# Performance work log

Hardware: AMD Instinct MI355X
Metric: run time of the kernel (lower is better)

Reference implementation:

```python
import jax, jax.numpy as jnp
import numpy as np

T = 2048
C = 2048
N_HEAD = 16
HEAD_DIM = C // N_HEAD


def setup_inputs() -> dict:
    key = jax.random.key(0)
    k1, k2, k3 = jax.random.split(key, 3)
    x = jax.random.normal(k1, (T, C), dtype=jnp.float32)
    # eqx.nn.Linear weight convention: (out_features, in_features)
    W_attn = jax.random.normal(k2, (3 * C, C), dtype=jnp.float32) * (1.0 / np.sqrt(C))
    W_proj = jax.random.normal(k3, (C, C), dtype=jnp.float32) * (1.0 / np.sqrt(C))
    return {"x": x, "W_attn": W_attn, "W_proj": W_proj}


def reference(x, W_attn, W_proj):
    # qkv projection: (T, 3C)
    qkv = x @ W_attn.T
    q, k, v = jnp.split(qkv, 3, axis=-1)
    # reshape to (H, T, d)
    q = q.reshape(T, N_HEAD, HEAD_DIM).transpose(1, 0, 2)
    k = k.reshape(T, N_HEAD, HEAD_DIM).transpose(1, 0, 2)
    v = v.reshape(T, N_HEAD, HEAD_DIM).transpose(1, 0, 2)
    # scaled causal attention: (H, T, T)
    att = jnp.einsum('htd,hsd->hts', q, k)
    causal_mask = jnp.triu(jnp.ones((T, T), dtype=bool), k=1)  # mask future keys
    att = jnp.where(causal_mask, -jnp.inf, att)
    att = jax.nn.softmax(att / jnp.sqrt(jnp.float32(HEAD_DIM)), axis=-1)
    # attention output: (H, T, d) -> (T, C)
    out = jnp.einsum('hts,hsd->htd', att, v)
    out = out.transpose(1, 0, 2).reshape(T, C)
    return out @ W_proj.T
```

## Files before the change

kernel.cpp:

```cpp
#include <hip/hip_runtime.h>
#include <cstdint>

using bx8 = __attribute__((ext_vector_type(8))) __bf16;
using us8 = __attribute__((ext_vector_type(8))) unsigned short;
using us4 = __attribute__((ext_vector_type(4))) unsigned short;
using fl8 = __attribute__((ext_vector_type(8))) float;
using fx4 = __attribute__((ext_vector_type(4))) float;

static __device__ inline unsigned short f2bf(float f) {
  unsigned u = __builtin_bit_cast(unsigned, f);
  unsigned r = 0x7FFFu + ((u >> 16) & 1u);
  return (unsigned short)((u + r) >> 16);
}
static __device__ inline float bf2f(unsigned short s) {
  return __builtin_bit_cast(float, (unsigned)s << 16);
}

static __device__ inline fx4 mfma16(bx8 a, bx8 b, fx4 c) {
  return __builtin_amdgcn_mfma_f32_16x16x32_bf16(a, b, c, 0, 0, 0);
}

static __device__ inline void gload16(const void* g, void* lds) {
  __builtin_amdgcn_global_load_lds(
      (const __attribute__((address_space(1))) void*)g,
      (__attribute__((address_space(3))) void*)lds,
      16, 0, 0);
}
#define VMCNT(n) asm volatile("s_waitcnt vmcnt(" #n ")" ::: "memory")
static __device__ inline void wave_barrier() {
  __builtin_amdgcn_sched_barrier(0);
  __builtin_amdgcn_s_barrier();
  __builtin_amdgcn_sched_barrier(0);
}
static __device__ inline void lds_barrier() {
  __builtin_amdgcn_sched_barrier(0);
  asm volatile("s_waitcnt lgkmcnt(0)" ::: "memory");
  __builtin_amdgcn_s_barrier();
  __builtin_amdgcn_sched_barrier(0);
}

#define DPP_ROR(x, k) __builtin_bit_cast(float, __builtin_amdgcn_update_dpp( \
    __builtin_bit_cast(int, x), __builtin_bit_cast(int, x), 0x120 | (k), 0xF, 0xF, false))

static __device__ inline float rowmax16(float v) {
  v = fmaxf(v, DPP_ROR(v, 1));
  v = fmaxf(v, DPP_ROR(v, 2));
  v = fmaxf(v, DPP_ROR(v, 4));
  v = fmaxf(v, DPP_ROR(v, 8));
  return v;
}
static __device__ inline float rowsum16(float v) {
  v += DPP_ROR(v, 1);
  v += DPP_ROR(v, 2);
  v += DPP_ROR(v, 4);
  v += DPP_ROR(v, 8);
  return v;
}

__global__ __launch_bounds__(256) void f2b_kernel(const float* __restrict__ in,
                                                  unsigned short* __restrict__ out,
                                                  int n) {
  int i = (blockIdx.x * 256 + threadIdx.x) * 4;
  if (i >= n) return;
  float4 v = *reinterpret_cast<const float4*>(in + i);
  ushort4 o;
  o.x = f2bf(v.x); o.y = f2bf(v.y); o.z = f2bf(v.z); o.w = f2bf(v.w);
  *reinterpret_cast<ushort4*>(out + i) = o;
}

__global__ __launch_bounds__(512, 2) void gemm256(const unsigned short* __restrict__ A,
                                                  const unsigned short* __restrict__ B,
                                                  unsigned short* __restrict__ C,
                                                  int M, int N, int K) {
  __shared__ unsigned short lds[4][2][256 * 32];

  const int tid = threadIdx.x;
  const int w = tid >> 6, l = tid & 63;
  const int l16 = l & 15, lg = l >> 4;
  const int wr = w >> 2, wc = w & 3;
  const long mb = (long)blockIdx.y * 256, nb = (long)blockIdx.x * 256;

  const int lr = l >> 2;
  const int sw = (((l & 3) ^ (lr & 3)) * 8);
  const unsigned short* Ag = A + (mb + w * 32 + lr) * (long)K + sw;
  const unsigned short* Bg = B + (nb + w * 32 + lr) * (long)K + sw;

  const int rdcol = ((lg ^ (l16 & 3)) * 16);

  const fx4 fz = {0.f, 0.f, 0.f, 0.f};
  fx4 acc[8][4];
#pragma unroll
  for (int i = 0; i < 8; ++i)
#pragma unroll
    for (int j = 0; j < 4; ++j) acc[i][j] = fz;

  const int nt = K >> 5;

  auto stage = [&](int tp) {
    const int db = tp & 3;
    const unsigned short* as = Ag + tp * 32;
    const unsigned short* bs = Bg + tp * 32;
    char* al = (char*)&lds[db][0][0] + w * 32 * 64;
    char* bl = (char*)&lds[db][1][0] + w * 32 * 64;
    gload16(as, al);
    gload16(as + 16 * (long)K, al + 1024);
    gload16(bs, bl);
    gload16(bs + 16 * (long)K, bl + 1024);
  };

  auto compute = [&](int bt) {
    const char* Ab = (const char*)&lds[bt][0][0] + (wr * 128 + l16) * 64 + rdcol;
    const char* Bb = (const char*)&lds[bt][1][0] + (wc * 64 + l16) * 64 + rdcol;
    bx8 bf[4];
#pragma unroll
    for (int nf = 0; nf < 4; ++nf)
      bf[nf] = *reinterpret_cast<const bx8*>(Bb + nf * 1024);
    __builtin_amdgcn_s_setprio(1);
#pragma unroll
    for (int mf = 0; mf < 8; ++mf) {
      bx8 av = *reinterpret_cast<const bx8*>(Ab + mf * 1024);
#pragma unroll
      for (int nf = 0; nf < 4; ++nf)
        acc[mf][nf] = mfma16(av, bf[nf], acc[mf][nf]);
    }
    __builtin_amdgcn_s_setprio(0);
  };

  stage(0); stage(1); stage(2);
  VMCNT(8);
  wave_barrier();

  int t = 0;
  for (; t < nt - 3; ++t) {
    stage(t + 3);
    compute(t & 3);
    VMCNT(8);
    wave_barrier();
  }
  compute(t & 3); VMCNT(4); wave_barrier(); ++t;
  compute(t & 3); VMCNT(0); wave_barrier(); ++t;
  compute(t & 3);

#pragma unroll
  for (int mf = 0; mf < 8; ++mf)
#pragma unroll
    for (int nf = 0; nf < 4; ++nf)
#pragma unroll
      for (int r = 0; r < 4; ++r) {
        const long row = mb + wr * 128 + mf * 16 + lg * 4 + r;
        const long col = nb + wc * 64 + nf * 16 + l16;
        C[row * N + col] = f2bf(acc[mf][nf][r]);
      }
}

template <typename T> struct RegOf { using type = us8; };
template <> struct RegOf<float>  { using type = fl8; };

template <typename T>
static __device__ inline typename RegOf<T>::type load8(const T* p) {
  return *reinterpret_cast<const typename RegOf<T>::type*>(p);
}
static __device__ inline us8 toBf(us8 v) { return v; }
static __device__ inline us8 toBf(fl8 f) {
  us8 o;
#pragma unroll
  for (int j = 0; j < 8; ++j) {
    __bf16 b = (__bf16)f[j];
    o[j] = __builtin_bit_cast(unsigned short, b);
  }
  return o;
}

template <typename TA, typename TB, bool F32OUT>
__global__ __launch_bounds__(256) void gemm_bt(const TA* __restrict__ A,
                                               const TB* __restrict__ B,
                                               void* __restrict__ Cp,
                                               int M, int N, int K) {
  __shared__ alignas(16) unsigned short As[128 * 64];
  __shared__ alignas(16) unsigned short Bs[128 * 64];
  const int tid = threadIdx.x;
  const int w = tid >> 6, l = tid & 63;
  const int l16 = l & 15, lg = l >> 4;
  const int wr = w >> 1, wc = w & 1;
  const long mb = (long)blockIdx.y * 128, nb = (long)blockIdx.x * 128;

  const fx4 fz = {0.f, 0.f, 0.f, 0.f};
  fx4 acc[4][4];
#pragma unroll
  for (int i = 0; i < 4; ++i)
#pragma unroll
    for (int j = 0; j < 4; ++j) acc[i][j] = fz;

  const int sr  = tid >> 3;
  const int sc8 = (tid & 7) * 8;
  const int wbc = sc8 * 2;

  typename RegOf<TA>::type rA[4];
  typename RegOf<TB>::type rB[4];

#pragma unroll
  for (int p = 0; p < 4; ++p) {
    const int row = p * 32 + sr;
    rA[p] = load8(A + (mb + row) * (long)K + sc8);
    rB[p] = load8(B + (nb + row) * (long)K + sc8);
  }

  for (int k0 = 0; k0 < K; k0 += 64) {
    lds_barrier();
#pragma unroll
    for (int p = 0; p < 4; ++p) {
      const int row = p * 32 + sr;
      const int eo = row * 64 + ((wbc ^ ((row & 7) << 4)) >> 1);
      *reinterpret_cast<us8*>(&As[eo]) = toBf(rA[p]);
      *reinterpret_cast<us8*>(&Bs[eo]) = toBf(rB[p]);
    }
    if (k0 + 64 < K) {
#pragma unroll
      for (int p = 0; p < 4; ++p) {
        const int row = p * 32 + sr;
        rA[p] = load8(A + (mb + row) * (long)K + k0 + 64 + sc8);
        rB[p] = load8(B + (nb + row) * (long)K + k0 + 64 + sc8);
      }
    }
    lds_barrier();
#pragma unroll
    for (int kk = 0; kk < 2; ++kk) {
      bx8 a[4], b[4];
#pragma unroll
      for (int mf = 0; mf < 4; ++mf) {
        const int ra = wr * 64 + mf * 16 + l16;
        const int bc = kk * 64 + lg * 16;
        a[mf] = *reinterpret_cast<const bx8*>(&As[ra * 64 + ((bc ^ ((ra & 7) << 4)) >> 1)]);
      }
#pragma unroll
      for (int nf = 0; nf < 4; ++nf) {
        const int rb_ = wc * 64 + nf * 16 + l16;
        const int bc = kk * 64 + lg * 16;
        b[nf] = *reinterpret_cast<const bx8*>(&Bs[rb_ * 64 + ((bc ^ ((rb_ & 7) << 4)) >> 1)]);
      }
#pragma unroll
      for (int mf = 0; mf < 4; ++mf)
#pragma unroll
        for (int nf = 0; nf < 4; ++nf)
          acc[mf][nf] = mfma16(a[mf], b[nf], acc[mf][nf]);
    }
  }

#pragma unroll
  for (int mf = 0; mf < 4; ++mf)
#pragma unroll
    for (int nf = 0; nf < 4; ++nf)
#pragma unroll
      for (int r = 0; r < 4; ++r) {
        const long row = mb + wr * 64 + mf * 16 + lg * 4 + r;
        const long col = nb + wc * 64 + nf * 16 + l16;
        if (F32OUT)
          ((float*)Cp)[row * N + col] = acc[mf][nf][r];
        else
          ((unsigned short*)Cp)[row * N + col] = f2bf(acc[mf][nf][r]);
      }
}

__global__ __launch_bounds__(256) void fa_kernel(const unsigned short* __restrict__ qkv,
                                                 unsigned short* __restrict__ Obuf,
                                                 float* __restrict__ ML) {
  __shared__ alignas(16) char smem[40960];

  const int id = blockIdx.x;
  const int h = id & 15, i = id >> 4;
  int qt, ck;
  if (i < 32)      { qt = 31 - (i >> 2); ck = i & 3; }
  else if (i < 56) { const int j = i - 32; qt = 23 - j / 3; ck = j % 3; }
  else if (i < 72) { const int j = i - 56; qt = 15 - (j >> 1); ck = j & 1; }
  else             { qt = 7 - (i - 72); ck = 0; }
  const int t0 = ck * 8;
  const int t1 = min(t0 + 8, qt + 1);
  const int qb = qt * 64;

  const int tid = threadIdx.x;
  const int w = tid >> 6, l = tid & 63;
  const int l16 = l & 15, lg = l >> 4;
  const fx4 fz = {0.f, 0.f, 0.f, 0.f};

  const int kr = tid >> 4, ksl = tid & 15;
  const int kg = tid & 15, db = tid >> 4;
  const int kc8 = ksl * 8;

  bx8 qf[4];
  {
    const long qrow = qb + w * 16 + l16;
    const unsigned short* qp = qkv + qrow * 6144L + h * 128 + lg * 8;
#pragma unroll
    for (int kc = 0; kc < 4; ++kc)
      qf[kc] = *reinterpret_cast<const bx8*>(qp + kc * 32);
  }

  fx4 o_acc[8];
#pragma unroll
  for (int i2 = 0; i2 < 8; ++i2) o_acc[i2] = fz;
  float m_r[4] = {-3e38f, -3e38f, -3e38f, -3e38f};
  float l_r[4] = {0.f, 0.f, 0.f, 0.f};

  us8 rK[4], rV[4];
  {
    const long kvb = (long)t0 * 64;
#pragma unroll
    for (int p = 0; p < 4; ++p)
      rK[p] = *reinterpret_cast<const us8*>(qkv + (kvb + p * 16 + kr) * 6144L + 2048 + h * 128 + kc8);
#pragma unroll
    for (int p = 0; p < 4; ++p)
      rV[p] = *reinterpret_cast<const us8*>(qkv + (kvb + kg * 4 + p) * 6144L + 4096 + h * 128 + db * 8);
  }

  const float sc2 = 0.1275173831f;
  char* const psb = smem + 32768 + w * 2048;

  for (int t = t0; t < t1; ++t) {
    lds_barrier();

#pragma unroll
    for (int p = 0; p < 4; ++p)
      *reinterpret_cast<us8*>(smem + (p * 16 + kr) * 256 + ((ksl ^ kr) << 4)) = rK[p];
#pragma unroll
    for (int j = 0; j < 8; ++j) {
      us4 vw = {rV[0][j], rV[1][j], rV[2][j], rV[3][j]};
      *reinterpret_cast<us4*>(smem + 16384 + (db * 8 + j) * 128 +
                              (((kg >> 1) ^ j) << 4) + ((kg & 1) << 3)) = vw;
    }

    if (t + 1 < t1) {
      const long kvb = (long)(t + 1) * 64;
#pragma unroll
      for (int p = 0; p < 4; ++p)
        rK[p] = *reinterpret_cast<const us8*>(qkv + (kvb + p * 16 + kr) * 6144L + 2048 + h * 128 + kc8);
#pragma unroll
      for (int p = 0; p < 4; ++p)
        rV[p] = *reinterpret_cast<const us8*>(qkv + (kvb + kg * 4 + p) * 6144L + 4096 + h * 128 + db * 8);
    }
    lds_barrier();

    fx4 s[4];
#pragma unroll
    for (int nf = 0; nf < 4; ++nf) s[nf] = fz;
#pragma unroll
    for (int kc = 0; kc < 4; ++kc) {
#pragma unroll
      for (int nf = 0; nf < 4; ++nf) {
        const int rl = nf * 16 + l16;
        bx8 kb = *reinterpret_cast<const bx8*>(smem + rl * 256 + (((kc * 4 + lg) ^ l16) << 4));
        s[nf] = mfma16(qf[kc], kb, s[nf]);
      }
    }

    if (t == qt) {
#pragma unroll
      for (int nf = 0; nf < 4; ++nf) {
        const int kv_abs = t * 64 + nf * 16 + l16;
#pragma unroll
        for (int r = 0; r < 4; ++r) {
          const int q_abs = qb + w * 16 + lg * 4 + r;
          if (kv_abs > q_abs) s[nf][r] = -3e38f;
        }
      }
    }

    float rm_[4];
    bool st = true;
#pragma unroll
    for (int r = 0; r < 4; ++r) {
      float rm = fmaxf(fmaxf(s[0][r], s[1][r]), fmaxf(s[2][r], s[3][r]));
      rm_[r] = rowmax16(rm);
      st = st && (rm_[r] - m_r[r] <= 62.7f);
    }
    float pv[4][4];
    if (__all(st ? 1 : 0)) {
#pragma unroll
      for (int r = 0; r < 4; ++r) {
        float rs = 0.f;
#pragma unroll
        for (int nf = 0; nf < 4; ++nf) {
          const float p = exp2f((s[nf][r] - m_r[r]) * sc2);
          pv[nf][r] = p;
          rs += p;
        }
        l_r[r] += rowsum16(rs);
      }
    } else {
#pragma unroll
      for (int r = 0; r < 4; ++r) {
        const float mn = fmaxf(m_r[r], rm_[r]);
        const float fac = exp2f((m_r[r] - mn) * sc2);
        m_r[r] = mn;
        float rs = 0.f;
#pragma unroll
        for (int nf = 0; nf < 4; ++nf) {
          const float p = exp2f((s[nf][r] - mn) * sc2);
          pv[nf][r] = p;
          rs += p;
        }
        l_r[r] = l_r[r] * fac + rowsum16(rs);
#pragma unroll
        for (int nf = 0; nf < 8; ++nf) o_acc[nf][r] *= fac;
      }
    }

#pragma unroll
    for (int nf = 0; nf < 4; ++nf)
#pragma unroll
      for (int r = 0; r < 4; ++r) {
        const int ro = lg * 4 + r;
        *reinterpret_cast<unsigned short*>(
            psb + ro * 128 + (((nf * 2 + (l16 >> 3)) ^ (ro & 7)) << 4) + ((l16 & 7) << 1)) =
            __builtin_bit_cast(unsigned short, (__bf16)pv[nf][r]);
      }

    bx8 pa[2];
#pragma unroll
    for (int kc = 0; kc < 2; ++kc)
      pa[kc] = *reinterpret_cast<const bx8*>(psb + l16 * 128 + (((kc * 4 + lg) ^ (l16 & 7)) << 4));

#pragma unroll
    for (int nf = 0; nf < 8; ++nf) {
#pragma unroll
      for (int kc = 0; kc < 2; ++kc) {
        bx8 vb = *reinterpret_cast<const bx8*>(smem + 16384 + (nf * 16 + l16) * 128 +
                                               (((kc * 4 + lg) ^ (l16 & 7)) << 4));
        o_acc[nf] = mfma16(pa[kc], vb, o_acc[nf]);
      }
    }
  }

  unsigned short* ob = Obuf + (long)id * 8192;
#pragma unroll
  for (int nf = 0; nf < 8; ++nf)
#pragma unroll
    for (int r = 0; r < 4; ++r) {
      const int row = w * 16 + lg * 4 + r;
      ob[row * 128 + nf * 16 + l16] = f2bf(o_acc[nf][r]);
    }
  if (l16 == 0) {
#pragma unroll
    for (int r = 0; r < 4; ++r) {
      const int row = w * 16 + lg * 4 + r;
      ML[((long)id * 64 + row) * 2 + 0] = m_r[r];
      ML[((long)id * 64 + row) * 2 + 1] = l_r[r];
    }
  }
}

__global__ __launch_bounds__(256) void fa_combine(const unsigned short* __restrict__ Obuf,
                                                  const float* __restrict__ ML,
                                                  unsigned short* __restrict__ out) {
  const int p = blockIdx.x;
  const int qt = p >> 4, h = p & 15;
  const int nc = (qt + 8) >> 3;
  const int tid = threadIdx.x;
  const int row = tid >> 2;
  const int c0 = (tid & 3) * 32;
  const float sc2 = 0.1275173831f;

  int ids[4];
#pragma unroll
  for (int k = 0; k < 4; ++k) {
    int ib;
    if (qt >= 24)      ib = (31 - qt) * 4 + k;
    else if (qt >= 16) ib = 32 + (23 - qt) * 3 + k;
    else if (qt >= 8)  ib = 56 + (15 - qt) * 2 + k;
    else               ib = 72 + (7 - qt);
    ids[k] = ib * 16 + h;
  }

  float mk[4], lk[4];
  float m = -3e38f;
#pragma unroll
  for (int k = 0; k < 4; ++k)
    if (k < nc) {
      mk[k] = ML[((long)ids[k] * 64 + row) * 2 + 0];
      lk[k] = ML[((long)ids[k] * 64 + row) * 2 + 1];
      m = fmaxf(m, mk[k]);
    }
  float fk[4], denom = 0.f;
#pragma unroll
  for (int k = 0; k < 4; ++k)
    if (k < nc) {
      fk[k] = exp2f((mk[k] - m) * sc2);
      denom += lk[k] * fk[k];
    }
  const float inv = 1.0f / denom;

  float acc[32];
#pragma unroll
  for (int j = 0; j < 32; ++j) acc[j] = 0.f;
#pragma unroll
  for (int k = 0; k < 4; ++k)
    if (k < nc) {
      const unsigned short* ob = Obuf + (long)ids[k] * 8192 + row * 128 + c0;
      const float f = fk[k];
#pragma unroll
      for (int jj = 0; jj < 4; ++jj) {
        us8 a = *reinterpret_cast<const us8*>(ob + jj * 8);
#pragma unroll
        for (int j2 = 0; j2 < 8; ++j2) acc[jj * 8 + j2] += bf2f(a[j2]) * f;
      }
    }

  unsigned short* dst = out + (long)(qt * 64 + row) * 2048 + h * 128 + c0;
#pragma unroll
  for (int jj = 0; jj < 4; ++jj) {
    ushort4 o0, o1;
    o0.x = f2bf(acc[jj * 8 + 0] * inv);
    o0.y = f2bf(acc[jj * 8 + 1] * inv);
    o0.z = f2bf(acc[jj * 8 + 2] * inv);
    o0.w = f2bf(acc[jj * 8 + 3] * inv);
    o1.x = f2bf(acc[jj * 8 + 4] * inv);
    o1.y = f2bf(acc[jj * 8 + 5] * inv);
    o1.z = f2bf(acc[jj * 8 + 6] * inv);
    o1.w = f2bf(acc[jj * 8 + 7] * inv);
    *reinterpret_cast<ushort4*>(dst + jj * 8) = o0;
    *reinterpret_cast<ushort4*>(dst + jj * 8 + 4) = o1;
  }
}

extern "C" void kernel_launch(void* const* d_in, const int* in_sizes, int n_in,
                              void* d_out, int out_size, void* d_ws, size_t ws_size,
                              hipStream_t stream) {
  const float* x  = (const float*)d_in[0];
  const float* Wa = (const float*)d_in[1];
  const float* Wp = (const float*)d_in[2];
  float* out = (float*)d_out;
  char* ws = (char*)d_ws;

  unsigned short* wab   = (unsigned short*)(ws);
  unsigned short* qkvb  = (unsigned short*)(ws + (24ull << 20));
  unsigned short* xb    = (unsigned short*)(ws + (48ull << 20));
  unsigned short* Obuf  = (unsigned short*)(ws);
  float*          ML    = (float*)(ws + (20ull << 20));
  unsigned short* attnb = (unsigned short*)(ws + (48ull << 20));

  f2b_kernel<<<4096, 256, 0, stream>>>(x, xb, 2048 * 2048);
  f2b_kernel<<<12288, 256, 0, stream>>>(Wa, wab, 6144 * 2048);

  gemm256<<<dim3(24, 8), 512, 0, stream>>>(xb, wab, qkvb, 2048, 6144, 2048);

  fa_kernel<<<1280, 256, 0, stream>>>(qkvb, Obuf, ML);

  fa_combine<<<512, 256, 0, stream>>>(Obuf, ML, attnb);

  gemm_bt<unsigned short, float, true><<<dim3(16, 16), 256, 0, stream>>>(attnb, Wp, (void*)out, 2048, 2048, 2048);
}
```

Baseline: 180.0 us.

## Pre-convert W_proj to bf16 and use async 4-stage LDS pipeline for output GEMM

Replaces the register-staged output projection GEMM, which converted fp32 weights inline, with a new kernel that streams bf16 tiles straight into LDS through global_load_lds. It uses a 4-deep buffer of 32-wide K slices, XOR-swizzled, and raises wave priority during the MFMA section. W_proj is converted to bf16 by a separate f2b pass into the workspace, which adds a launch and extra memory traffic. The aim is to hide global load latency and halve the weight bytes the GEMM reads.

```diff
diff --git a/kernel.cpp b/kernel.cpp
--- a/kernel.cpp
+++ b/kernel.cpp
@@ -153,37 +153,25 @@
       }
 }
 
-template <typename T> struct RegOf { using type = us8; };
-template <> struct RegOf<float>  { using type = fl8; };
-
-template <typename T>
-static __device__ inline typename RegOf<T>::type load8(const T* p) {
-  return *reinterpret_cast<const typename RegOf<T>::type*>(p);
-}
-static __device__ inline us8 toBf(us8 v) { return v; }
-static __device__ inline us8 toBf(fl8 f) {
-  us8 o;
-#pragma unroll
-  for (int j = 0; j < 8; ++j) {
-    __bf16 b = (__bf16)f[j];
-    o[j] = __builtin_bit_cast(unsigned short, b);
-  }
-  return o;
-}
-
-template <typename TA, typename TB, bool F32OUT>
-__global__ __launch_bounds__(256) void gemm_bt(const TA* __restrict__ A,
-                                               const TB* __restrict__ B,
-                                               void* __restrict__ Cp,
-                                               int M, int N, int K) {
-  __shared__ alignas(16) unsigned short As[128 * 64];
-  __shared__ alignas(16) unsigned short Bs[128 * 64];
+__global__ __launch_bounds__(256) void gemm2p(const unsigned short* __restrict__ A,
+                                              const unsigned short* __restrict__ B,
+                                              float* __restrict__ C,
+                                              int M, int N, int K) {
+  __shared__ unsigned short lds[4][2][128 * 32];
+
   const int tid = threadIdx.x;
   const int w = tid >> 6, l = tid & 63;
   const int l16 = l & 15, lg = l >> 4;
   const int wr = w >> 1, wc = w & 1;
   const long mb = (long)blockIdx.y * 128, nb = (long)blockIdx.x * 128;
 
+  const int lr = l >> 2;
+  const int sw = (((l & 3) ^ (lr & 3)) * 8);
+  const unsigned short* Ag = A + (mb + w * 32 + lr) * (long)K + sw;
+  const unsigned short* Bg = B + (nb + w * 32 + lr) * (long)K + sw;
+
+  const int rdcol = ((lg ^ (l16 & 3)) * 16);
+
   const fx4 fz = {0.f, 0.f, 0.f, 0.f};
   fx4 acc[4][4];
 #pragma unroll
@@ -191,60 +179,52 @@
 #pragma unroll
     for (int j = 0; j < 4; ++j) acc[i][j] = fz;
 
-  const int sr  = tid >> 3;
-  const int sc8 = (tid & 7) * 8;
-  const int wbc = sc8 * 2;
-
-  typename RegOf<TA>::type rA[4];
-  typename RegOf<TB>::type rB[4];
-
-#pragma unroll
-  for (int p = 0; p < 4; ++p) {
-    const int row = p * 32 + sr;
-    rA[p] = load8(A + (mb + row) * (long)K + sc8);
-    rB[p] = load8(B + (nb + row) * (long)K + sc8);
-  }
-
-  for (int k0 = 0; k0 < K; k0 += 64) {
-    lds_barrier();
-#pragma unroll
-    for (int p = 0; p < 4; ++p) {
-      const int row = p * 32 + sr;
-      const int eo = row * 64 + ((wbc ^ ((row & 7) << 4)) >> 1);
-      *reinterpret_cast<us8*>(&As[eo]) = toBf(rA[p]);
-      *reinterpret_cast<us8*>(&Bs[eo]) = toBf(rB[p]);
-    }
-    if (k0 + 64 < K) {
-#pragma unroll
-      for (int p = 0; p < 4; ++p) {
-        const int row = p * 32 + sr;
-        rA[p] = load8(A + (mb + row) * (long)K + k0 + 64 + sc8);
-        rB[p] = load8(B + (nb + row) * (long)K + k0 + 64 + sc8);
-      }
-    }
-    lds_barrier();
-#pragma unroll
-    for (int kk = 0; kk < 2; ++kk) {
-      bx8 a[4], b[4];
-#pragma unroll
-      for (int mf = 0; mf < 4; ++mf) {
-        const int ra = wr * 64 + mf * 16 + l16;
-        const int bc = kk * 64 + lg * 16;
-        a[mf] = *reinterpret_cast<const bx8*>(&As[ra * 64 + ((bc ^ ((ra & 7) << 4)) >> 1)]);
-      }
-#pragma unroll
-      for (int nf = 0; nf < 4; ++nf) {
-        const int rb_ = wc * 64 + nf * 16 + l16;
-        const int bc = kk * 64 + lg * 16;
-        b[nf] = *reinterpret_cast<const bx8*>(&Bs[rb_ * 64 + ((bc ^ ((rb_ & 7) << 4)) >> 1)]);
-      }
-#pragma unroll
-      for (int mf = 0; mf < 4; ++mf)
-#pragma unroll
-        for (int nf = 0; nf < 4; ++nf)
-          acc[mf][nf] = mfma16(a[mf], b[nf], acc[mf][nf]);
-    }
-  }
+  const int nt = K >> 5;
+
+  auto stage = [&](int tp) {
+    const int db = tp & 3;
+    const unsigned short* as = Ag + tp * 32;
+    const unsigned short* bs = Bg + tp * 32;
+    char* al = (char*)&lds[db][0][0] + w * 32 * 64;
+    char* bl = (char*)&lds[db][1][0] + w * 32 * 64;
+    gload16(as, al);
+    gload16(as + 16 * (long)K, al + 1024);
+    gload16(bs, bl);
+    gload16(bs + 16 * (long)K, bl + 1024);
+  };
+
+  auto compute = [&](int bt) {
+    const char* Ab = (const char*)&lds[bt][0][0] + (wr * 64 + l16) * 64 + rdcol;
+    const char* Bb = (const char*)&lds[bt][1][0] + (wc * 64 + l16) * 64 + rdcol;
+    bx8 bf[4];
+#pragma unroll
+    for (int nf = 0; nf < 4; ++nf)
+      bf[nf] = *reinterpret_cast<const bx8*>(Bb + nf * 1024);
+    __builtin_amdgcn_s_setprio(1);
+#pragma unroll
+    for (int mf = 0; mf < 4; ++mf) {
+      bx8 av = *reinterpret_cast<const bx8*>(Ab + mf * 1024);
+#pragma unroll
+      for (int nf = 0; nf < 4; ++nf)
+        acc[mf][nf] = mfma16(av, bf[nf], acc[mf][nf]);
+    }
+    __builtin_amdgcn_s_setprio(0);
+  };
+
+  stage(0); stage(1); stage(2);
+  VMCNT(8);
+  wave_barrier();
+
+  int t = 0;
+  for (; t < nt - 3; ++t) {
+    stage(t + 3);
+    compute(t & 3);
+    VMCNT(8);
+    wave_barrier();
+  }
+  compute(t & 3); VMCNT(4); wave_barrier(); ++t;
+  compute(t & 3); VMCNT(0); wave_barrier(); ++t;
+  compute(t & 3);
 
 #pragma unroll
   for (int mf = 0; mf < 4; ++mf)
@@ -254,10 +234,7 @@
       for (int r = 0; r < 4; ++r) {
         const long row = mb + wr * 64 + mf * 16 + lg * 4 + r;
         const long col = nb + wc * 64 + nf * 16 + l16;
-        if (F32OUT)
-          ((float*)Cp)[row * N + col] = acc[mf][nf][r];
-        else
-          ((unsigned short*)Cp)[row * N + col] = f2bf(acc[mf][nf][r]);
+        C[row * N + col] = acc[mf][nf][r];
       }
 }
 
@@ -536,6 +513,7 @@
   unsigned short* Obuf  = (unsigned short*)(ws);
   float*          ML    = (float*)(ws + (20ull << 20));
   unsigned short* attnb = (unsigned short*)(ws + (48ull << 20));
+  unsigned short* wpb   = (unsigned short*)(ws);
 
   f2b_kernel<<<4096, 256, 0, stream>>>(x, xb, 2048 * 2048);
   f2b_kernel<<<12288, 256, 0, stream>>>(Wa, wab, 6144 * 2048);
@@ -546,5 +524,7 @@
 
   fa_combine<<<512, 256, 0, stream>>>(Obuf, ML, attnb);
 
-  gemm_bt<unsigned short, float, true><<<dim3(16, 16), 256, 0, stream>>>(attnb, Wp, (void*)out, 2048, 2048, 2048);
-}
+  f2b_kernel<<<4096, 256, 0, stream>>>(Wp, wpb, 2048 * 2048);
+
+  gemm2p<<<dim3(16, 16), 256, 0, stream>>>(attnb, wpb, out, 2048, 2048, 2048);
+}
```

New measurement: 183.8 us. 2.1% more time.
